# Kernel optimization log

Measured on AMD Instinct MI355X. Metric: run time of the kernel, lower is better.

## Reference

```python
import jax, jax.numpy as jnp
import numpy as np

S, P, C = 64, 2048, 32   # num_scenes, num_pixels, scene_channels
A, D, E = 2048, 128, 64  # agent_size, dynamics_features, embed_dim


def setup_inputs() -> dict:
    key = jax.random.key(0)
    ks = jax.random.split(key, 9)
    inv = lambda n: 1.0 / np.sqrt(n)
    return {
        "global_scene": jax.random.normal(ks[0], (S, P, C), jnp.float32),
        "scene_idx": jax.random.randint(ks[1], (A,), 0, S),
        "dynamic_encoding": jax.random.normal(ks[2], (A, D), jnp.float32),
        "W_sn": jax.random.uniform(ks[3], (C, E), jnp.float32, -inv(C), inv(C)),
        "b_sn": jax.random.uniform(ks[4], (E,), jnp.float32, -inv(C), inv(C)),
        "W_df": jax.random.uniform(ks[5], (D, E), jnp.float32, -inv(D), inv(D)),
        "b_df": jax.random.uniform(ks[6], (E,), jnp.float32, -inv(D), inv(D)),
        "w_fc": jax.random.uniform(ks[7], (E,), jnp.float32, -inv(E), inv(E)),
        "b_fc": jax.random.uniform(ks[8], (1,), jnp.float32, -inv(E), inv(E)),
    }


def reference(global_scene, scene_idx, dynamic_encoding, W_sn, b_sn, W_df, b_df, w_fc, b_fc):
    # att1: [S, P, E]; att2: [A, E]
    att1 = jnp.einsum('spc,ce->spe', global_scene, W_sn) + b_sn
    att2 = dynamic_encoding @ W_df + b_df
    # gather scenes per agent, fuse add + relu: [A, P, E]
    add_fusion = jax.nn.relu(att1[scene_idx] + att2[:, None, :])
    # linear to scalar score per pixel, softmax over pixels (dim=1)
    logits = jnp.einsum('ape,e->ap', add_fusion, w_fc) + b_fc[0]  # [A, P]
    alpha = jax.nn.softmax(logits, axis=1)[:, :, None]            # [A, P, 1]
    # alpha-weighted pooling of gathered scene features -> [A, C]
    return jnp.sum(alpha * global_scene[scene_idx], axis=1)
```

## Files before the change

### kernel.cpp

```cpp
#include <hip/hip_runtime.h>
#include <hip/hip_bf16.h>

#define S_ 64
#define P_ 2048
#define C_ 32
#define A_ 2048
#define D_ 128
#define E_ 64

#define LPX   64
#define NLCH  (P_ / LPX)
#define PPC   128
#define NPCH  (P_ / PPC)

__global__ __launch_bounds__(256) void att2_kernel(
    const float* __restrict__ de, const float* __restrict__ Wdf,
    const float* __restrict__ bdf, float* __restrict__ att2) {
  __shared__ float4 Wl[128 * 16];
  __shared__ float4 bl[16];
  __shared__ float  dl[16 * 128];
  const int tid = threadIdx.x;

  const float4* W4 = (const float4*)Wdf;
#pragma unroll
  for (int i = 0; i < 8; ++i) Wl[tid + i * 256] = W4[tid + i * 256];
  if (tid < 16) bl[tid] = ((const float4*)bdf)[tid];
  const long base = (long)blockIdx.x * (16 * 128);
#pragma unroll
  for (int i = 0; i < 8; ++i) dl[tid + i * 256] = de[base + tid + i * 256];
  __syncthreads();

  const int r = tid >> 4, e4 = tid & 15;
  float4 acc = bl[e4];
#pragma unroll 4
  for (int d = 0; d < 128; ++d) {
    const float  g = dl[r * 128 + d];
    const float4 w = Wl[d * 16 + e4];
    acc.x = fmaf(g, w.x, acc.x);
    acc.y = fmaf(g, w.y, acc.y);
    acc.z = fmaf(g, w.z, acc.z);
    acc.w = fmaf(g, w.w, acc.w);
  }
  ((float4*)att2)[((long)blockIdx.x * 16 + r) * 16 + e4] = acc;
}

__global__ void scatter_kernel(const int* __restrict__ sidx,
                               int* __restrict__ counts, int* __restrict__ lists) {
  const int a = blockIdx.x * 256 + threadIdx.x;
  const int s = sidx[a];
  const int pos = atomicAdd(&counts[s], 1);
  lists[s * A_ + pos] = a;
}

__global__ __launch_bounds__(256) void logits_kernel(
    const float* __restrict__ gs, const float* __restrict__ Wsn,
    const float* __restrict__ bsn, const float* __restrict__ wfc,
    const float* __restrict__ att2, const int* __restrict__ counts,
    const int* __restrict__ lists, float* __restrict__ logits) {
  const int s   = blockIdx.x >> 5;
  const int p0  = (blockIdx.x & (NLCH - 1)) * LPX;
  const int tid = threadIdx.x;
  const int px  = tid >> 2;
  const int eq  = tid & 3;

  __shared__ float  gsl[LPX][33];
  __shared__ float4 Wl4[32 * 16];
  __shared__ float4 a2l[32][16];
  __shared__ int    aidl[32];

  const float4* W4 = (const float4*)Wsn;
  Wl4[tid]       = W4[tid];
  Wl4[tid + 256] = W4[tid + 256];

  const float4* g4 = (const float4*)(gs + ((long)s * P_ + p0) * C_);
#pragma unroll
  for (int k = 0; k < 2; ++k) {
    const int f = tid + k * 256;
    const float4 v = g4[f];
    const int pp = f >> 3, c0 = (f & 7) * 4;
    gsl[pp][c0]     = v.x;
    gsl[pp][c0 + 1] = v.y;
    gsl[pp][c0 + 2] = v.z;
    gsl[pp][c0 + 3] = v.w;
  }

  const float4* wf4 = (const float4*)wfc;
  const float4* b4  = (const float4*)bsn;
  float4 wf[4], a1[4];
#pragma unroll
  for (int q = 0; q < 4; ++q) { wf[q] = wf4[eq * 4 + q]; a1[q] = b4[eq * 4 + q]; }
  __syncthreads();

#pragma unroll
  for (int c = 0; c < 32; ++c) {
    const float g = gsl[px][c];
#pragma unroll
    for (int q = 0; q < 4; ++q) {
      const float4 w = Wl4[c * 16 + eq * 4 + q];
      a1[q].x = fmaf(g, w.x, a1[q].x);
      a1[q].y = fmaf(g, w.y, a1[q].y);
      a1[q].z = fmaf(g, w.z, a1[q].z);
      a1[q].w = fmaf(g, w.w, a1[q].w);
    }
  }

  const int n_s = counts[s];
  for (int g0 = 0; g0 < n_s; g0 += 32) {
    const int m = min(32, n_s - g0);
    __syncthreads();
    if (tid < m) aidl[tid] = lists[s * A_ + g0 + tid];
    __syncthreads();
#pragma unroll
    for (int k = 0; k < 2; ++k) {
      const int idx = tid + k * 256;
      const int j = idx >> 4, e4 = idx & 15;
      if (j < m) a2l[j][e4] = ((const float4*)att2)[aidl[j] * 16 + e4];
    }
    __syncthreads();

    for (int j = 0; j < m; ++j) {
      const float4 t0 = a2l[j][eq * 4 + 0];
      const float4 t1 = a2l[j][eq * 4 + 1];
      const float4 t2 = a2l[j][eq * 4 + 2];
      const float4 t3 = a2l[j][eq * 4 + 3];
      float c0 = 0.f, c1 = 0.f, c2 = 0.f, c3 = 0.f;
      c0 = fmaf(fmaxf(a1[0].x + t0.x, 0.f), wf[0].x, c0);
      c1 = fmaf(fmaxf(a1[0].y + t0.y, 0.f), wf[0].y, c1);
      c2 = fmaf(fmaxf(a1[0].z + t0.z, 0.f), wf[0].z, c2);
      c3 = fmaf(fmaxf(a1[0].w + t0.w, 0.f), wf[0].w, c3);
      c0 = fmaf(fmaxf(a1[1].x + t1.x, 0.f), wf[1].x, c0);
      c1 = fmaf(fmaxf(a1[1].y + t1.y, 0.f), wf[1].y, c1);
      c2 = fmaf(fmaxf(a1[1].z + t1.z, 0.f), wf[1].z, c2);
      c3 = fmaf(fmaxf(a1[1].w + t1.w, 0.f), wf[1].w, c3);
      c0 = fmaf(fmaxf(a1[2].x + t2.x, 0.f), wf[2].x, c0);
      c1 = fmaf(fmaxf(a1[2].y + t2.y, 0.f), wf[2].y, c1);
      c2 = fmaf(fmaxf(a1[2].z + t2.z, 0.f), wf[2].z, c2);
      c3 = fmaf(fmaxf(a1[2].w + t2.w, 0.f), wf[2].w, c3);
      c0 = fmaf(fmaxf(a1[3].x + t3.x, 0.f), wf[3].x, c0);
      c1 = fmaf(fmaxf(a1[3].y + t3.y, 0.f), wf[3].y, c1);
      c2 = fmaf(fmaxf(a1[3].z + t3.z, 0.f), wf[3].z, c2);
      c3 = fmaf(fmaxf(a1[3].w + t3.w, 0.f), wf[3].w, c3);
      float r = (c0 + c1) + (c2 + c3);
      r += __shfl_xor(r, 1);
      r += __shfl_xor(r, 2);
      if (eq == 0) logits[(long)aidl[j] * P_ + p0 + px] = r;
    }
  }
}

__global__ __launch_bounds__(256) void stats_kernel(
    const float* __restrict__ logits, float2* __restrict__ stats) {
  const int a = blockIdx.x, tid = threadIdx.x;
  __shared__ float red[8];
  const float4* l4 = (const float4*)(logits + (long)a * P_);
  const float4 v0 = l4[tid], v1 = l4[tid + 256];
  float m = fmaxf(fmaxf(fmaxf(v0.x, v0.y), fmaxf(v0.z, v0.w)),
                  fmaxf(fmaxf(v1.x, v1.y), fmaxf(v1.z, v1.w)));
#pragma unroll
  for (int off = 1; off < 64; off <<= 1) m = fmaxf(m, __shfl_xor(m, off));
  if ((tid & 63) == 0) red[tid >> 6] = m;
  __syncthreads();
  m = fmaxf(fmaxf(red[0], red[1]), fmaxf(red[2], red[3]));

  float sum = __expf(v0.x - m) + __expf(v0.y - m) + __expf(v0.z - m) + __expf(v0.w - m)
            + __expf(v1.x - m) + __expf(v1.y - m) + __expf(v1.z - m) + __expf(v1.w - m);
#pragma unroll
  for (int off = 1; off < 64; off <<= 1) sum += __shfl_xor(sum, off);
  if ((tid & 63) == 0) red[4 + (tid >> 6)] = sum;
  __syncthreads();
  if (tid == 0) {
    const float Z = red[4] + red[5] + red[6] + red[7];
    stats[a] = make_float2(m, 1.0f / Z);
  }
}

__global__ __launch_bounds__(256) void pool_kernel(
    const float* __restrict__ logits, const float2* __restrict__ stats,
    const int* __restrict__ counts, const int* __restrict__ lists,
    const float* __restrict__ gs, float* __restrict__ out) {
  const int s   = blockIdx.x >> 4;
  const int p0  = (blockIdx.x & (NPCH - 1)) * PPC;
  const int tid = threadIdx.x;
  const int j   = tid >> 3;
  const int c4  = tid & 7;

  __shared__ float4 gsl[PPC][8];
  __shared__ float  alpha_l[32][132];
  __shared__ float2 sm[32];
  __shared__ int    aid[32];

  const float4* g4 = (const float4*)(gs + ((long)s * P_ + p0) * C_);
  float4* gl = (float4*)gsl;
#pragma unroll
  for (int k = 0; k < 4; ++k) gl[tid + k * 256] = g4[tid + k * 256];

  const float4* l4 = (const float4*)logits;
  const int n_s = counts[s];

  for (int g0 = 0; g0 < n_s; g0 += 32) {
    const int m = min(32, n_s - g0);
    __syncthreads();
    if (tid < m) {
      const int a = lists[s * A_ + g0 + tid];
      aid[tid] = a;
      sm[tid]  = stats[a];
    }
    __syncthreads();

#pragma unroll
    for (int k = 0; k < 4; ++k) {
      const int idx = tid + k * 256;
      const int jj = idx >> 5, p4 = idx & 31;
      if (jj < m) {
        const float2 ms = sm[jj];
        const float4 v  = l4[(long)aid[jj] * (P_ / 4) + (p0 >> 2) + p4];
        float4 al;
        al.x = __expf(v.x - ms.x) * ms.y;
        al.y = __expf(v.y - ms.x) * ms.y;
        al.z = __expf(v.z - ms.x) * ms.y;
        al.w = __expf(v.w - ms.x) * ms.y;
        ((float4*)&alpha_l[jj][0])[p4] = al;
      }
    }
    __syncthreads();

    if (j < m) {
      float4 a0 = make_float4(0.f, 0.f, 0.f, 0.f);
      float4 a1 = make_float4(0.f, 0.f, 0.f, 0.f);
      float4 a2 = make_float4(0.f, 0.f, 0.f, 0.f);
      float4 a3 = make_float4(0.f, 0.f, 0.f, 0.f);
#pragma unroll 4
      for (int p4 = 0; p4 < PPC / 4; ++p4) {
        const float4 aw = ((const float4*)&alpha_l[j][0])[p4];
        const float4 v0 = gsl[p4 * 4 + 0][c4];
        const float4 v1 = gsl[p4 * 4 + 1][c4];
        const float4 v2 = gsl[p4 * 4 + 2][c4];
        const float4 v3 = gsl[p4 * 4 + 3][c4];
        a0.x = fmaf(aw.x, v0.x, a0.x); a0.y = fmaf(aw.x, v0.y, a0.y);
        a0.z = fmaf(aw.x, v0.z, a0.z); a0.w = fmaf(aw.x, v0.w, a0.w);
        a1.x = fmaf(aw.y, v1.x, a1.x); a1.y = fmaf(aw.y, v1.y, a1.y);
        a1.z = fmaf(aw.y, v1.z, a1.z); a1.w = fmaf(aw.y, v1.w, a1.w);
        a2.x = fmaf(aw.z, v2.x, a2.x); a2.y = fmaf(aw.z, v2.y, a2.y);
        a2.z = fmaf(aw.z, v2.z, a2.z); a2.w = fmaf(aw.z, v2.w, a2.w);
        a3.x = fmaf(aw.w, v3.x, a3.x); a3.y = fmaf(aw.w, v3.y, a3.y);
        a3.z = fmaf(aw.w, v3.z, a3.z); a3.w = fmaf(aw.w, v3.w, a3.w);
      }
      const float4 acc = make_float4((a0.x + a1.x) + (a2.x + a3.x),
                                     (a0.y + a1.y) + (a2.y + a3.y),
                                     (a0.z + a1.z) + (a2.z + a3.z),
                                     (a0.w + a1.w) + (a2.w + a3.w));
      float* op = out + (long)aid[j] * C_ + c4 * 4;
      atomicAdd(op,     acc.x);
      atomicAdd(op + 1, acc.y);
      atomicAdd(op + 2, acc.z);
      atomicAdd(op + 3, acc.w);
    }
  }
}

extern "C" void kernel_launch(void* const* d_in, const int* in_sizes, int n_in,
                              void* d_out, int out_size, void* d_ws, size_t ws_size,
                              hipStream_t stream) {
  const float* gs   = (const float*)d_in[0];
  const int*   sidx = (const int*)  d_in[1];
  const float* de   = (const float*)d_in[2];
  const float* Wsn  = (const float*)d_in[3];
  const float* bsn  = (const float*)d_in[4];
  const float* Wdf  = (const float*)d_in[5];
  const float* bdf  = (const float*)d_in[6];
  const float* wfc  = (const float*)d_in[7];
  float* out = (float*)d_out;

  float*  att2   = (float*)d_ws;
  float*  logits = att2 + (long)A_ * E_;
  float2* stats  = (float2*)(logits + (long)A_ * P_);
  int*    counts = (int*)(stats + A_);
  int*    lists  = counts + 64;

  hipMemsetAsync(counts, 0, 64 * sizeof(int), stream);
  hipMemsetAsync(out, 0, (size_t)out_size * sizeof(float), stream);

  att2_kernel   <<<A_ / 16,    256, 0, stream>>>(de, Wdf, bdf, att2);
  scatter_kernel<<<A_ / 256,   256, 0, stream>>>(sidx, counts, lists);
  logits_kernel <<<S_ * NLCH,  256, 0, stream>>>(gs, Wsn, bsn, wfc, att2,
                                                 counts, lists, logits);
  stats_kernel  <<<A_,         256, 0, stream>>>(logits, stats);
  pool_kernel   <<<S_ * NPCH,  256, 0, stream>>>(logits, stats, counts,
                                                 lists, gs, out);
}
```

Before: 158.7 us.

## Fuse logits, softmax and pooling into one kernel using unnormalized exp weights

```diff
diff --git a/kernel.cpp b/kernel.cpp
--- a/kernel.cpp
+++ b/kernel.cpp
@@ -10,16 +10,23 @@
 
 #define LPX   64
 #define NLCH  (P_ / LPX)
-#define PPC   128
-#define NPCH  (P_ / PPC)
-
-__global__ __launch_bounds__(256) void att2_kernel(
+
+__global__ __launch_bounds__(256) void att2s_kernel(
     const float* __restrict__ de, const float* __restrict__ Wdf,
-    const float* __restrict__ bdf, float* __restrict__ att2) {
+    const float* __restrict__ bdf, const int* __restrict__ sidx,
+    float* __restrict__ att2, int* __restrict__ counts,
+    int* __restrict__ lists) {
   __shared__ float4 Wl[128 * 16];
   __shared__ float4 bl[16];
   __shared__ float  dl[16 * 128];
   const int tid = threadIdx.x;
+
+  if (tid < 16) {
+    const int a = blockIdx.x * 16 + tid;
+    const int s = sidx[a];
+    const int pos = atomicAdd(&counts[s], 1);
+    lists[s * A_ + pos] = a;
+  }
 
   const float4* W4 = (const float4*)Wdf;
 #pragma unroll
@@ -44,28 +51,22 @@
   ((float4*)att2)[((long)blockIdx.x * 16 + r) * 16 + e4] = acc;
 }
 
-__global__ void scatter_kernel(const int* __restrict__ sidx,
-                               int* __restrict__ counts, int* __restrict__ lists) {
-  const int a = blockIdx.x * 256 + threadIdx.x;
-  const int s = sidx[a];
-  const int pos = atomicAdd(&counts[s], 1);
-  lists[s * A_ + pos] = a;
-}
-
-__global__ __launch_bounds__(256) void logits_kernel(
+__global__ __launch_bounds__(256) void fused_kernel(
     const float* __restrict__ gs, const float* __restrict__ Wsn,
     const float* __restrict__ bsn, const float* __restrict__ wfc,
     const float* __restrict__ att2, const int* __restrict__ counts,
-    const int* __restrict__ lists, float* __restrict__ logits) {
+    const int* __restrict__ lists, float* __restrict__ out,
+    float* __restrict__ Z) {
   const int s   = blockIdx.x >> 5;
   const int p0  = (blockIdx.x & (NLCH - 1)) * LPX;
   const int tid = threadIdx.x;
   const int px  = tid >> 2;
   const int eq  = tid & 3;
 
-  __shared__ float  gsl[LPX][33];
+  __shared__ float  gsl[LPX][36];
   __shared__ float4 Wl4[32 * 16];
   __shared__ float4 a2l[32][16];
+  __shared__ float  alpha_l[32][64];
   __shared__ int    aidl[32];
 
   const float4* W4 = (const float4*)Wsn;
@@ -104,7 +105,10 @@
     }
   }
 
+  const int j2 = tid >> 3;
+  const int c4 = tid & 7;
   const int n_s = counts[s];
+
   for (int g0 = 0; g0 < n_s; g0 += 32) {
     const int m = min(32, n_s - g0);
     __syncthreads();
@@ -143,119 +147,55 @@
       float r = (c0 + c1) + (c2 + c3);
       r += __shfl_xor(r, 1);
       r += __shfl_xor(r, 2);
-      if (eq == 0) logits[(long)aidl[j] * P_ + p0 + px] = r;
-    }
-  }
-}
-
-__global__ __launch_bounds__(256) void stats_kernel(
-    const float* __restrict__ logits, float2* __restrict__ stats) {
-  const int a = blockIdx.x, tid = threadIdx.x;
-  __shared__ float red[8];
-  const float4* l4 = (const float4*)(logits + (long)a * P_);
-  const float4 v0 = l4[tid], v1 = l4[tid + 256];
-  float m = fmaxf(fmaxf(fmaxf(v0.x, v0.y), fmaxf(v0.z, v0.w)),
-                  fmaxf(fmaxf(v1.x, v1.y), fmaxf(v1.z, v1.w)));
-#pragma unroll
-  for (int off = 1; off < 64; off <<= 1) m = fmaxf(m, __shfl_xor(m, off));
-  if ((tid & 63) == 0) red[tid >> 6] = m;
-  __syncthreads();
-  m = fmaxf(fmaxf(red[0], red[1]), fmaxf(red[2], red[3]));
-
-  float sum = __expf(v0.x - m) + __expf(v0.y - m) + __expf(v0.z - m) + __expf(v0.w - m)
-            + __expf(v1.x - m) + __expf(v1.y - m) + __expf(v1.z - m) + __expf(v1.w - m);
-#pragma unroll
-  for (int off = 1; off < 64; off <<= 1) sum += __shfl_xor(sum, off);
-  if ((tid & 63) == 0) red[4 + (tid >> 6)] = sum;
-  __syncthreads();
-  if (tid == 0) {
-    const float Z = red[4] + red[5] + red[6] + red[7];
-    stats[a] = make_float2(m, 1.0f / Z);
-  }
-}
-
-__global__ __launch_bounds__(256) void pool_kernel(
-    const float* __restrict__ logits, const float2* __restrict__ stats,
-    const int* __restrict__ counts, const int* __restrict__ lists,
-    const float* __restrict__ gs, float* __restrict__ out) {
-  const int s   = blockIdx.x >> 4;
-  const int p0  = (blockIdx.x & (NPCH - 1)) * PPC;
-  const int tid = threadIdx.x;
-  const int j   = tid >> 3;
-  const int c4  = tid & 7;
-
-  __shared__ float4 gsl[PPC][8];
-  __shared__ float  alpha_l[32][132];
-  __shared__ float2 sm[32];
-  __shared__ int    aid[32];
-
-  const float4* g4 = (const float4*)(gs + ((long)s * P_ + p0) * C_);
-  float4* gl = (float4*)gsl;
-#pragma unroll
-  for (int k = 0; k < 4; ++k) gl[tid + k * 256] = g4[tid + k * 256];
-
-  const float4* l4 = (const float4*)logits;
-  const int n_s = counts[s];
-
-  for (int g0 = 0; g0 < n_s; g0 += 32) {
-    const int m = min(32, n_s - g0);
-    __syncthreads();
-    if (tid < m) {
-      const int a = lists[s * A_ + g0 + tid];
-      aid[tid] = a;
-      sm[tid]  = stats[a];
-    }
-    __syncthreads();
-
-#pragma unroll
-    for (int k = 0; k < 4; ++k) {
-      const int idx = tid + k * 256;
-      const int jj = idx >> 5, p4 = idx & 31;
-      if (jj < m) {
-        const float2 ms = sm[jj];
-        const float4 v  = l4[(long)aid[jj] * (P_ / 4) + (p0 >> 2) + p4];
-        float4 al;
-        al.x = __expf(v.x - ms.x) * ms.y;
-        al.y = __expf(v.y - ms.x) * ms.y;
-        al.z = __expf(v.z - ms.x) * ms.y;
-        al.w = __expf(v.w - ms.x) * ms.y;
-        ((float4*)&alpha_l[jj][0])[p4] = al;
+      if (eq == 0) alpha_l[j][px] = __expf(r);
+    }
+    __syncthreads();
+
+    if (j2 < m) {
+      const int a = aidl[j2];
+      float4 a0 = make_float4(0.f, 0.f, 0.f, 0.f);
+      float4 a1p = make_float4(0.f, 0.f, 0.f, 0.f);
+      float4 a2p = make_float4(0.f, 0.f, 0.f, 0.f);
+      float4 a3p = make_float4(0.f, 0.f, 0.f, 0.f);
+      float  zs = 0.f;
+#pragma unroll 4
+      for (int p4 = 0; p4 < LPX / 4; ++p4) {
+        const float w0 = alpha_l[j2][p4 * 4 + 0];
+        const float w1 = alpha_l[j2][p4 * 4 + 1];
+        const float w2 = alpha_l[j2][p4 * 4 + 2];
+        const float w3 = alpha_l[j2][p4 * 4 + 3];
+        const float4 v0 = *(const float4*)&gsl[p4 * 4 + 0][c4 * 4];
+        const float4 v1 = *(const float4*)&gsl[p4 * 4 + 1][c4 * 4];
+        const float4 v2 = *(const float4*)&gsl[p4 * 4 + 2][c4 * 4];
+        const float4 v3 = *(const float4*)&gsl[p4 * 4 + 3][c4 * 4];
+        zs += (w0 + w1) + (w2 + w3);
+        a0.x = fmaf(w0, v0.x, a0.x); a0.y = fmaf(w0, v0.y, a0.y);
+        a0.z = fmaf(w0, v0.z, a0.z); a0.w = fmaf(w0, v0.w, a0.w);
+        a1p.x = fmaf(w1, v1.x, a1p.x); a1p.y = fmaf(w1, v1.y, a1p.y);
+        a1p.z = fmaf(w1, v1.z, a1p.z); a1p.w = fmaf(w1, v1.w, a1p.w);
+        a2p.x = fmaf(w2, v2.x, a2p.x); a2p.y = fmaf(w2, v2.y, a2p.y);
+        a2p.z = fmaf(w2, v2.z, a2p.z); a2p.w = fmaf(w2, v2.w, a2p.w);
+        a3p.x = fmaf(w3, v3.x, a3p.x); a3p.y = fmaf(w3, v3.y, a3p.y);
+        a3p.z = fmaf(w3, v3.z, a3p.z); a3p.w = fmaf(w3, v3.w, a3p.w);
       }
-    }
-    __syncthreads();
-
-    if (j < m) {
-      float4 a0 = make_float4(0.f, 0.f, 0.f, 0.f);
-      float4 a1 = make_float4(0.f, 0.f, 0.f, 0.f);
-      float4 a2 = make_float4(0.f, 0.f, 0.f, 0.f);
-      float4 a3 = make_float4(0.f, 0.f, 0.f, 0.f);
-#pragma unroll 4
-      for (int p4 = 0; p4 < PPC / 4; ++p4) {
-        const float4 aw = ((const float4*)&alpha_l[j][0])[p4];
-        const float4 v0 = gsl[p4 * 4 + 0][c4];
-        const float4 v1 = gsl[p4 * 4 + 1][c4];
-        const float4 v2 = gsl[p4 * 4 + 2][c4];
-        const float4 v3 = gsl[p4 * 4 + 3][c4];
-        a0.x = fmaf(aw.x, v0.x, a0.x); a0.y = fmaf(aw.x, v0.y, a0.y);
-        a0.z = fmaf(aw.x, v0.z, a0.z); a0.w = fmaf(aw.x, v0.w, a0.w);
-        a1.x = fmaf(aw.y, v1.x, a1.x); a1.y = fmaf(aw.y, v1.y, a1.y);
-        a1.z = fmaf(aw.y, v1.z, a1.z); a1.w = fmaf(aw.y, v1.w, a1.w);
-        a2.x = fmaf(aw.z, v2.x, a2.x); a2.y = fmaf(aw.z, v2.y, a2.y);
-        a2.z = fmaf(aw.z, v2.z, a2.z); a2.w = fmaf(aw.z, v2.w, a2.w);
-        a3.x = fmaf(aw.w, v3.x, a3.x); a3.y = fmaf(aw.w, v3.y, a3.y);
-        a3.z = fmaf(aw.w, v3.z, a3.z); a3.w = fmaf(aw.w, v3.w, a3.w);
-      }
-      const float4 acc = make_float4((a0.x + a1.x) + (a2.x + a3.x),
-                                     (a0.y + a1.y) + (a2.y + a3.y),
-                                     (a0.z + a1.z) + (a2.z + a3.z),
-                                     (a0.w + a1.w) + (a2.w + a3.w));
-      float* op = out + (long)aid[j] * C_ + c4 * 4;
+      const float4 acc = make_float4((a0.x + a1p.x) + (a2p.x + a3p.x),
+                                     (a0.y + a1p.y) + (a2p.y + a3p.y),
+                                     (a0.z + a1p.z) + (a2p.z + a3p.z),
+                                     (a0.w + a1p.w) + (a2p.w + a3p.w));
+      float* op = out + (long)a * C_ + c4 * 4;
       atomicAdd(op,     acc.x);
       atomicAdd(op + 1, acc.y);
       atomicAdd(op + 2, acc.z);
       atomicAdd(op + 3, acc.w);
-    }
-  }
+      if (c4 == 0) atomicAdd(&Z[a], zs);
+    }
+  }
+}
+
+__global__ __launch_bounds__(256) void norm_kernel(
+    float* __restrict__ out, const float* __restrict__ Z) {
+  const int i = blockIdx.x * 256 + threadIdx.x;
+  out[i] = out[i] / Z[i >> 5];
 }
 
 extern "C" void kernel_launch(void* const* d_in, const int* in_sizes, int n_in,
@@ -271,20 +211,17 @@
   const float* wfc  = (const float*)d_in[7];
   float* out = (float*)d_out;
 
-  float*  att2   = (float*)d_ws;
-  float*  logits = att2 + (long)A_ * E_;
-  float2* stats  = (float2*)(logits + (long)A_ * P_);
-  int*    counts = (int*)(stats + A_);
-  int*    lists  = counts + 64;
-
-  hipMemsetAsync(counts, 0, 64 * sizeof(int), stream);
+  float* att2   = (float*)d_ws;
+  float* Z      = att2 + (long)A_ * E_;
+  int*   counts = (int*)(Z + A_);
+  int*   lists  = counts + 64;
+
+  hipMemsetAsync(Z, 0, (A_ + 64) * sizeof(float), stream);
   hipMemsetAsync(out, 0, (size_t)out_size * sizeof(float), stream);
 
-  att2_kernel   <<<A_ / 16,    256, 0, stream>>>(de, Wdf, bdf, att2);
-  scatter_kernel<<<A_ / 256,   256, 0, stream>>>(sidx, counts, lists);
-  logits_kernel <<<S_ * NLCH,  256, 0, stream>>>(gs, Wsn, bsn, wfc, att2,
-                                                 counts, lists, logits);
-  stats_kernel  <<<A_,         256, 0, stream>>>(logits, stats);
-  pool_kernel   <<<S_ * NPCH,  256, 0, stream>>>(logits, stats, counts,
-                                                 lists, gs, out);
-}
+  att2s_kernel<<<A_ / 16,   256, 0, stream>>>(de, Wdf, bdf, sidx, att2,
+                                              counts, lists);
+  fused_kernel<<<S_ * NLCH, 256, 0, stream>>>(gs, Wsn, bsn, wfc, att2,
+                                              counts, lists, out, Z);
+  norm_kernel <<<(A_ * C_) / 256, 256, 0, stream>>>(out, Z);
+}
```

New measurement: 161.9 us. +2.0%, slower.
